# Optimization experiments

Measured on AMD Instinct MI355X. Metric: run time of the kernel, lower is better.

The kernel has to match this reference:

```python
import jax, jax.numpy as jnp
import numpy as np

EPS = 1e-7  # keras.backend.epsilon()


def setup_inputs() -> dict:
    key = jax.random.key(0)
    k1, k2, k3 = jax.random.split(key, 3)
    B, N, D_in, C, D_out = 32, 2048, 8, 32, 16
    x = jax.random.normal(k1, (B, N, D_in), dtype=jnp.float32)
    W = jax.random.normal(k2, (1, N, C, D_out, D_in), dtype=jnp.float32) * 0.05
    R = jax.random.normal(k3, (1, N, C), dtype=jnp.float32)
    return {"x": x, "W": W, "R": R}


def reference(x, W, R):
    # x: [B, N, D_in]; W: [1, N, C, D_out, D_in]; R: [1, N, C]
    R_nor = jax.nn.softmax(R[0], axis=0)          # softmax over N (axis=1 of [1,N,C])
    # per-capsule transform: u[b,n,c,j] = sum_k W[n,c,j,k] * x[b,n,k]
    u = jnp.einsum('ncjk,bnk->bncj', W[0], x)
    # routing-weighted aggregation over input capsules n
    s = jnp.einsum('bncj,nc->bcj', u, R_nor)      # [B, C, D_out]
    # squash along capsule dim (original axis=-2 before squeeze == D_out)
    ss = jnp.sum(jnp.square(s), axis=-1, keepdims=True) + EPS
    scale = jnp.sqrt(ss) / (1.0 + ss)
    return scale * s                               # [B, C, D_out]
```

## Files before the change

### kernel.cpp

```cpp
#include <hip/hip_runtime.h>
#include <math.h>


#define NN 2048
#define CC 32
#define JJ 16
#define KK 8
#define BB 32

__global__ void caps_softmax(const float* __restrict__ R, float* __restrict__ Rn) {
  const int c = blockIdx.x;
  const int t = threadIdx.x;
  __shared__ float col[NN];
  __shared__ float red[256];

  float m = -INFINITY;
  for (int n = t; n < NN; n += 256) {
    float v = R[(size_t)n * CC + c];
    col[n] = v;
    m = fmaxf(m, v);
  }
  red[t] = m;
  __syncthreads();
  for (int h = 128; h >= 1; h >>= 1) {
    if (t < h) red[t] = fmaxf(red[t], red[t + h]);
    __syncthreads();
  }
  m = red[0];
  __syncthreads();

  float ssum = 0.f;
  for (int n = t; n < NN; n += 256) {
    float e = expf(col[n] - m);
    col[n] = e;
    ssum += e;
  }
  red[t] = ssum;
  __syncthreads();
  for (int h = 128; h >= 1; h >>= 1) {
    if (t < h) red[t] += red[t + h];
    __syncthreads();
  }
  float inv = 1.0f / red[0];
  for (int n = t; n < NN; n += 256) {
    Rn[(size_t)n * CC + c] = col[n] * inv;
  }
}

__device__ __forceinline__ void g2l16(const float* g, float* l) {
  __builtin_amdgcn_global_load_lds((const __attribute__((address_space(1))) void*)g,
                                   (__attribute__((address_space(3))) void*)l, 16, 0, 0);
}

__global__ void __launch_bounds__(512) caps_main(const float* __restrict__ x,
                                                 const float* __restrict__ W,
                                                 const float* __restrict__ Rn,
                                                 float* __restrict__ P) {
  const int bid = blockIdx.x;
  const int cg = bid & 3;
  const int chunk = bid >> 2;
  const int n0 = chunk * 32;
  const int tid = threadIdx.x;
  const int ws = tid >> 6;
  const int lane = tid & 63;
  const int j = lane & 15;
  const int bo = lane >> 4;

  extern __shared__ float smem[];
  float* ldsW = smem;
  float* ldsX = smem + 16384;

  float acc[8][8];
#pragma unroll
  for (int a = 0; a < 8; ++a)
#pragma unroll
    for (int b = 0; b < 8; ++b) acc[a][b] = 0.f;

  const int xs_nl = tid >> 6;
  const int xs_bi = (tid >> 3) & 7;
  const int xs_bo = (tid >> 1) & 3;
  const int xs_h  = tid & 1;
  const int xs_b  = xs_bo * 8 + xs_bi;

  {
    const int sbase = n0;
#pragma unroll
    for (int it = 0; it < 4; ++it) {
      int G = it * 512 + tid;
      int nl = G >> 8, q = G & 255;
      int qs = q ^ ((q >> 3) & 1);
      g2l16(W + (size_t)(sbase + nl) * 4096 + cg * 1024 + qs * 4,
            ldsW + (size_t)(it * 512 + ws * 64) * 4);
    }
    g2l16(x + (size_t)xs_b * (NN * KK) + (size_t)(sbase + xs_nl) * KK + xs_h * 4,
          ldsX + (size_t)ws * 256);
  }
  __syncthreads();

  const int xw = (j >> 2) & 1;
  const int jo_lo = j * 8 + xw * 4;
  const int jo_hi = j * 8 + (xw ^ 1) * 4;

  for (int s = 0; s < 4; ++s) {
    const int cur = s & 1;
    if (s < 3) {
      const int nxt = cur ^ 1;
      const int sbase = n0 + (s + 1) * 8;
#pragma unroll
      for (int it = 0; it < 4; ++it) {
        int G = it * 512 + tid;
        int nl = G >> 8, q = G & 255;
        int qs = q ^ ((q >> 3) & 1);
        g2l16(W + (size_t)(sbase + nl) * 4096 + cg * 1024 + qs * 4,
              ldsW + (size_t)nxt * 8192 + (size_t)(it * 512 + ws * 64) * 4);
      }
      g2l16(x + (size_t)xs_b * (NN * KK) + (size_t)(sbase + xs_nl) * KK + xs_h * 4,
            ldsX + (size_t)nxt * 2048 + (size_t)ws * 256);
    }
    {
      const int nglob = n0 + s * 8 + ws;
      const float* Xb = ldsX + (size_t)cur * 2048 + (size_t)ws * 256;
      const float* Wb = ldsW + (size_t)cur * 8192 + (size_t)ws * 1024;

      float xa[8][8];
#pragma unroll
      for (int bi = 0; bi < 8; ++bi) {
        float4 lo = *(const float4*)(Xb + bi * 32 + bo * 8);
        float4 hi = *(const float4*)(Xb + bi * 32 + bo * 8 + 4);
        xa[bi][0] = lo.x; xa[bi][1] = lo.y; xa[bi][2] = lo.z; xa[bi][3] = lo.w;
        xa[bi][4] = hi.x; xa[bi][5] = hi.y; xa[bi][6] = hi.z; xa[bi][7] = hi.w;
      }
      const float* rrow = Rn + (size_t)nglob * CC + cg * 8;
#pragma unroll
      for (int ci = 0; ci < 8; ++ci) {
        float4 wa = *(const float4*)(Wb + ci * 128 + jo_lo);
        float4 wb = *(const float4*)(Wb + ci * 128 + jo_hi);
        float rv = rrow[ci];
        float w0 = wa.x * rv, w1 = wa.y * rv, w2 = wa.z * rv, w3 = wa.w * rv;
        float w4 = wb.x * rv, w5 = wb.y * rv, w6 = wb.z * rv, w7 = wb.w * rv;
#pragma unroll
        for (int bi = 0; bi < 8; ++bi) {
          float a = acc[bi][ci];
          a = fmaf(w0, xa[bi][0], a);
          a = fmaf(w1, xa[bi][1], a);
          a = fmaf(w2, xa[bi][2], a);
          a = fmaf(w3, xa[bi][3], a);
          a = fmaf(w4, xa[bi][4], a);
          a = fmaf(w5, xa[bi][5], a);
          a = fmaf(w6, xa[bi][6], a);
          a = fmaf(w7, xa[bi][7], a);
          acc[bi][ci] = a;
        }
      }
    }
    __syncthreads();
  }

  float* red = smem;
#pragma unroll
  for (int half = 4; half >= 1; half >>= 1) {
    if (ws >= half && ws < 2 * half) {
      float* dst = red + (size_t)(ws - half) * 4096;
#pragma unroll
      for (int bi = 0; bi < 8; ++bi)
#pragma unroll
        for (int ci = 0; ci < 8; ++ci)
          dst[(bi * 8 + ci) * 64 + lane] = acc[bi][ci];
    }
    __syncthreads();
    if (ws < half) {
      const float* srcp = red + (size_t)ws * 4096;
#pragma unroll
      for (int bi = 0; bi < 8; ++bi)
#pragma unroll
        for (int ci = 0; ci < 8; ++ci)
          acc[bi][ci] += srcp[(bi * 8 + ci) * 64 + lane];
    }
    __syncthreads();
  }

  if (ws == 0) {
    float* dst = P + (size_t)bid * 4096;
#pragma unroll
    for (int bi = 0; bi < 8; ++bi)
#pragma unroll
      for (int ci = 0; ci < 8; ++ci)
        dst[(bi * 8 + ci) * 64 + lane] = acc[bi][ci];
  }
}

__global__ void caps_reduce(const float* __restrict__ P, float* __restrict__ out) {
  const int g = blockIdx.x * 256 + threadIdx.x;
  const int j = g & 15;
  const int c = (g >> 4) & 31;
  const int b = g >> 9;
  const int bo = b >> 3, bi = b & 7;
  const int cgi = c >> 3, ci = c & 7;
  const int idx = (bi * 8 + ci) * 64 + (bo * 16 + j);

  float s = 0.f;
  for (int chunk = 0; chunk < 64; ++chunk) {
    s += P[(size_t)(chunk * 4 + cgi) * 4096 + idx];
  }
  float sq = s * s;
  sq += __shfl_xor(sq, 8, 16);
  sq += __shfl_xor(sq, 4, 16);
  sq += __shfl_xor(sq, 2, 16);
  sq += __shfl_xor(sq, 1, 16);
  float ss = sq + 1e-7f;
  float scale = sqrtf(ss) / (1.0f + ss);
  out[g] = scale * s;
}

extern "C" void kernel_launch(void* const* d_in, const int* in_sizes, int n_in,
                              void* d_out, int out_size, void* d_ws, size_t ws_size,
                              hipStream_t stream) {
  const float* x = (const float*)d_in[0];
  const float* W = (const float*)d_in[1];
  const float* R = (const float*)d_in[2];
  float* out = (float*)d_out;

  float* Rn = (float*)d_ws;
  float* P  = (float*)d_ws + 65536;

  hipFuncSetAttribute((const void*)caps_main,
                      hipFuncAttributeMaxDynamicSharedMemorySize, 81920);

  caps_softmax<<<32, 256, 0, stream>>>(R, Rn);
  caps_main<<<256, 512, 81920, stream>>>(x, W, Rn, P);
  caps_reduce<<<64, 256, 0, stream>>>(P, out);
}
```

Baseline: 32.18 us.

## Fuse softmax normalization into main kernel and load W directly to registers

The softmax kernel now only computes the per-column max and inverse sum, and the main kernel recomputes the normalized routing weights with expf inline, which removes the write and read of the normalized matrix. The main kernel drops the double-buffered LDS staging of W. Each wave instead reads its W slices straight from global memory into registers, and all x for the chunk is staged into LDS once up front. This cuts shared-memory traffic and synchronisation, at the cost of no explicit prefetch overlap for W loads and extra exp work per block.

```diff
diff --git a/kernel.cpp b/kernel.cpp
--- a/kernel.cpp
+++ b/kernel.cpp
@@ -8,18 +8,19 @@
 #define KK 8
 #define BB 32
 
-__global__ void caps_softmax(const float* __restrict__ R, float* __restrict__ Rn) {
+__global__ void caps_stats(const float* __restrict__ R, float* __restrict__ M,
+                           float* __restrict__ I) {
   const int c = blockIdx.x;
   const int t = threadIdx.x;
-  __shared__ float col[NN];
   __shared__ float red[256];
 
-  float m = -INFINITY;
-  for (int n = t; n < NN; n += 256) {
-    float v = R[(size_t)n * CC + c];
-    col[n] = v;
-    m = fmaxf(m, v);
-  }
+  float v[8];
+#pragma unroll
+  for (int i = 0; i < 8; ++i) v[i] = R[(size_t)(t + i * 256) * CC + c];
+
+  float m = v[0];
+#pragma unroll
+  for (int i = 1; i < 8; ++i) m = fmaxf(m, v[i]);
   red[t] = m;
   __syncthreads();
   for (int h = 128; h >= 1; h >>= 1) {
@@ -29,21 +30,18 @@
   m = red[0];
   __syncthreads();
 
-  float ssum = 0.f;
-  for (int n = t; n < NN; n += 256) {
-    float e = expf(col[n] - m);
-    col[n] = e;
-    ssum += e;
-  }
-  red[t] = ssum;
+  float s = 0.f;
+#pragma unroll
+  for (int i = 0; i < 8; ++i) s += expf(v[i] - m);
+  red[t] = s;
   __syncthreads();
   for (int h = 128; h >= 1; h >>= 1) {
     if (t < h) red[t] += red[t + h];
     __syncthreads();
   }
-  float inv = 1.0f / red[0];
-  for (int n = t; n < NN; n += 256) {
-    Rn[(size_t)n * CC + c] = col[n] * inv;
+  if (t == 0) {
+    M[c] = m;
+    I[c] = 1.0f / red[0];
   }
 }
 
@@ -54,7 +52,9 @@
 
 __global__ void __launch_bounds__(512) caps_main(const float* __restrict__ x,
                                                  const float* __restrict__ W,
-                                                 const float* __restrict__ Rn,
+                                                 const float* __restrict__ R,
+                                                 const float* __restrict__ M,
+                                                 const float* __restrict__ I,
                                                  float* __restrict__ P) {
   const int bid = blockIdx.x;
   const int cg = bid & 3;
@@ -67,8 +67,24 @@
   const int bo = lane >> 4;
 
   extern __shared__ float smem[];
-  float* ldsW = smem;
-  float* ldsX = smem + 16384;
+  float* ldsX = smem;
+
+#pragma unroll
+  for (int it = 0; it < 4; ++it) {
+    int G = it * 512 + tid;
+    int nl = G >> 6, r = G & 63;
+    int bi = r >> 3, bo2 = (r >> 1) & 3, h = r & 1;
+    int b = bo2 * 8 + bi;
+    g2l16(x + (size_t)b * (NN * KK) + (size_t)(n0 + nl) * KK + h * 4,
+          ldsX + (size_t)(it * 512 + ws * 64) * 4);
+  }
+
+  float mC[8], ivC[8];
+#pragma unroll
+  for (int ci = 0; ci < 8; ++ci) {
+    mC[ci] = M[cg * 8 + ci];
+    ivC[ci] = I[cg * 8 + ci];
+  }
 
   float acc[8][8];
 #pragma unroll
@@ -76,86 +92,61 @@
 #pragma unroll
     for (int b = 0; b < 8; ++b) acc[a][b] = 0.f;
 
-  const int xs_nl = tid >> 6;
-  const int xs_bi = (tid >> 3) & 7;
-  const int xs_bo = (tid >> 1) & 3;
-  const int xs_h  = tid & 1;
-  const int xs_b  = xs_bo * 8 + xs_bi;
-
-  {
-    const int sbase = n0;
-#pragma unroll
-    for (int it = 0; it < 4; ++it) {
-      int G = it * 512 + tid;
-      int nl = G >> 8, q = G & 255;
-      int qs = q ^ ((q >> 3) & 1);
-      g2l16(W + (size_t)(sbase + nl) * 4096 + cg * 1024 + qs * 4,
-            ldsW + (size_t)(it * 512 + ws * 64) * 4);
-    }
-    g2l16(x + (size_t)xs_b * (NN * KK) + (size_t)(sbase + xs_nl) * KK + xs_h * 4,
-          ldsX + (size_t)ws * 256);
-  }
-  __syncthreads();
-
-  const int xw = (j >> 2) & 1;
-  const int jo_lo = j * 8 + xw * 4;
-  const int jo_hi = j * 8 + (xw ^ 1) * 4;
-
-  for (int s = 0; s < 4; ++s) {
-    const int cur = s & 1;
-    if (s < 3) {
-      const int nxt = cur ^ 1;
-      const int sbase = n0 + (s + 1) * 8;
-#pragma unroll
-      for (int it = 0; it < 4; ++it) {
-        int G = it * 512 + tid;
-        int nl = G >> 8, q = G & 255;
-        int qs = q ^ ((q >> 3) & 1);
-        g2l16(W + (size_t)(sbase + nl) * 4096 + cg * 1024 + qs * 4,
-              ldsW + (size_t)nxt * 8192 + (size_t)(it * 512 + ws * 64) * 4);
+  __syncthreads();
+
+  const float4* wb4base =
+      (const float4*)(W + (size_t)(n0 + ws * 4) * 4096 + cg * 1024 + j * 8);
+
+#pragma unroll 1
+  for (int nl = 0; nl < 4; ++nl) {
+    const int n = n0 + ws * 4 + nl;
+
+    const float4* wb4 = wb4base + (size_t)nl * 1024;
+    float4 wv[16];
+#pragma unroll
+    for (int ci = 0; ci < 8; ++ci) {
+      wv[2 * ci] = wb4[ci * 32];
+      wv[2 * ci + 1] = wb4[ci * 32 + 1];
+    }
+
+    const float* Xb = ldsX + (size_t)(ws * 4 + nl) * 256;
+    float xa[8][8];
+#pragma unroll
+    for (int bi = 0; bi < 8; ++bi) {
+      float4 lo = *(const float4*)(Xb + bi * 32 + bo * 8);
+      float4 hi = *(const float4*)(Xb + bi * 32 + bo * 8 + 4);
+      xa[bi][0] = lo.x; xa[bi][1] = lo.y; xa[bi][2] = lo.z; xa[bi][3] = lo.w;
+      xa[bi][4] = hi.x; xa[bi][5] = hi.y; xa[bi][6] = hi.z; xa[bi][7] = hi.w;
+    }
+
+    const float* rr = R + (size_t)n * CC + cg * 8;
+    float rv[8];
+#pragma unroll
+    for (int ci = 0; ci < 8; ++ci) rv[ci] = expf(rr[ci] - mC[ci]) * ivC[ci];
+
+#pragma unroll
+    for (int ci = 0; ci < 8; ++ci) {
+      float4 wa = wv[2 * ci], wb = wv[2 * ci + 1];
+      float rvv = rv[ci];
+      float w0 = wa.x * rvv, w1 = wa.y * rvv, w2 = wa.z * rvv, w3 = wa.w * rvv;
+      float w4 = wb.x * rvv, w5 = wb.y * rvv, w6 = wb.z * rvv, w7 = wb.w * rvv;
+#pragma unroll
+      for (int bi = 0; bi < 8; ++bi) {
+        float a = acc[bi][ci];
+        a = fmaf(w0, xa[bi][0], a);
+        a = fmaf(w1, xa[bi][1], a);
+        a = fmaf(w2, xa[bi][2], a);
+        a = fmaf(w3, xa[bi][3], a);
+        a = fmaf(w4, xa[bi][4], a);
+        a = fmaf(w5, xa[bi][5], a);
+        a = fmaf(w6, xa[bi][6], a);
+        a = fmaf(w7, xa[bi][7], a);
+        acc[bi][ci] = a;
       }
-      g2l16(x + (size_t)xs_b * (NN * KK) + (size_t)(sbase + xs_nl) * KK + xs_h * 4,
-            ldsX + (size_t)nxt * 2048 + (size_t)ws * 256);
-    }
-    {
-      const int nglob = n0 + s * 8 + ws;
-      const float* Xb = ldsX + (size_t)cur * 2048 + (size_t)ws * 256;
-      const float* Wb = ldsW + (size_t)cur * 8192 + (size_t)ws * 1024;
-
-      float xa[8][8];
-#pragma unroll
-      for (int bi = 0; bi < 8; ++bi) {
-        float4 lo = *(const float4*)(Xb + bi * 32 + bo * 8);
-        float4 hi = *(const float4*)(Xb + bi * 32 + bo * 8 + 4);
-        xa[bi][0] = lo.x; xa[bi][1] = lo.y; xa[bi][2] = lo.z; xa[bi][3] = lo.w;
-        xa[bi][4] = hi.x; xa[bi][5] = hi.y; xa[bi][6] = hi.z; xa[bi][7] = hi.w;
-      }
-      const float* rrow = Rn + (size_t)nglob * CC + cg * 8;
-#pragma unroll
-      for (int ci = 0; ci < 8; ++ci) {
-        float4 wa = *(const float4*)(Wb + ci * 128 + jo_lo);
-        float4 wb = *(const float4*)(Wb + ci * 128 + jo_hi);
-        float rv = rrow[ci];
-        float w0 = wa.x * rv, w1 = wa.y * rv, w2 = wa.z * rv, w3 = wa.w * rv;
-        float w4 = wb.x * rv, w5 = wb.y * rv, w6 = wb.z * rv, w7 = wb.w * rv;
-#pragma unroll
-        for (int bi = 0; bi < 8; ++bi) {
-          float a = acc[bi][ci];
-          a = fmaf(w0, xa[bi][0], a);
-          a = fmaf(w1, xa[bi][1], a);
-          a = fmaf(w2, xa[bi][2], a);
-          a = fmaf(w3, xa[bi][3], a);
-          a = fmaf(w4, xa[bi][4], a);
-          a = fmaf(w5, xa[bi][5], a);
-          a = fmaf(w6, xa[bi][6], a);
-          a = fmaf(w7, xa[bi][7], a);
-          acc[bi][ci] = a;
-        }
-      }
-    }
-    __syncthreads();
-  }
-
+    }
+  }
+
+  __syncthreads();
   float* red = smem;
 #pragma unroll
   for (int half = 4; half >= 1; half >>= 1) {
@@ -199,6 +190,7 @@
   const int idx = (bi * 8 + ci) * 64 + (bo * 16 + j);
 
   float s = 0.f;
+#pragma unroll
   for (int chunk = 0; chunk < 64; ++chunk) {
     s += P[(size_t)(chunk * 4 + cgi) * 4096 + idx];
   }
@@ -220,13 +212,14 @@
   const float* R = (const float*)d_in[2];
   float* out = (float*)d_out;
 
-  float* Rn = (float*)d_ws;
-  float* P  = (float*)d_ws + 65536;
+  float* M = (float*)d_ws;
+  float* I = (float*)d_ws + 32;
+  float* P = (float*)d_ws + 64;
 
   hipFuncSetAttribute((const void*)caps_main,
-                      hipFuncAttributeMaxDynamicSharedMemorySize, 81920);
-
-  caps_softmax<<<32, 256, 0, stream>>>(R, Rn);
-  caps_main<<<256, 512, 81920, stream>>>(x, W, Rn, P);
+                      hipFuncAttributeMaxDynamicSharedMemorySize, 65536);
+
+  caps_stats<<<32, 256, 0, stream>>>(R, M, I);
+  caps_main<<<256, 512, 65536, stream>>>(x, W, R, M, I, P);
   caps_reduce<<<64, 256, 0, stream>>>(P, out);
 }
```

Result: slower. 45.39 us (+41.1%).
